# Kernel optimization log

Measured on AMD Instinct MI355X. Metric: run time of the kernel, lower is better.

The kernel has to match this reference:

```python
import jax, jax.numpy as jnp
import numpy as np

T, D, H, E, K = 4096, 1024, 2048, 8, 2  # tokens, model dim, expert hidden, n_experts, top_k
AUX_COEF = 0.01


def setup_inputs() -> dict:
    key = jax.random.key(0)
    ks = jax.random.split(key, 8)
    sd = lambda fan_in: 1.0 / np.sqrt(fan_in)
    x = jax.random.normal(ks[0], (T, D), jnp.float32)
    Wr = jax.random.normal(ks[1], (E, D), jnp.float32) * sd(D)      # router (no bias)
    w1 = jax.random.normal(ks[2], (E, H, D), jnp.float32) * sd(D)   # stacked up-proj
    w2 = jax.random.normal(ks[3], (E, D, H), jnp.float32) * sd(H)   # stacked down-proj
    w3 = jax.random.normal(ks[4], (E, H, D), jnp.float32) * sd(D)   # stacked gate-proj
    w1s = jax.random.normal(ks[5], (H, D), jnp.float32) * sd(D)     # shared expert
    w2s = jax.random.normal(ks[6], (D, H), jnp.float32) * sd(H)
    w3s = jax.random.normal(ks[7], (H, D), jnp.float32) * sd(D)
    return dict(x=x, Wr=Wr, w1=w1, w2=w2, w3=w3, w1s=w1s, w2s=w2s, w3s=w3s)


def _gelu(v):
    return jax.nn.gelu(v, approximate=False)  # torch F.gelu default = exact erf


def reference(x, Wr, w1, w2, w3, w1s, w2s, w3s):
    n_tok = x.shape[0]
    router_out = x @ Wr.T                                   # [T, E]
    router_probs = jax.nn.softmax(router_out, axis=-1)
    _, topk_idx = jax.lax.top_k(router_out, K)              # [T, K]
    topk_probs, _ = jax.lax.top_k(router_probs, K)          # top-k of probs (same order)

    # auxiliary load-balance loss (first-choice density * mean prob)
    expert_mask = jax.nn.one_hot(topk_idx[:, 0], E, dtype=jnp.float32)
    density = expert_mask.mean(axis=0)
    aux_loss = AUX_COEF * jnp.sum(density * router_probs.mean(axis=0)) * E

    # combine weights C[t, e] = sum of routed probs for expert e at token t
    C = jnp.zeros((n_tok, E), x.dtype).at[
        jnp.arange(n_tok)[:, None], topk_idx
    ].add(topk_probs)

    # dense per-expert SwiGLU-style FFN, combined by C (equal math to
    # sort-based dispatch + scatter_add in the original)
    h = _gelu(jnp.einsum('td,ehd->teh', x, w1)) * jnp.einsum('td,ehd->teh', x, w3)
    ye = jnp.einsum('teh,edh->ted', h, w2)                  # [T, E, D]
    out = jnp.einsum('ted,te->td', ye, C)

    # shared expert (always active)
    out = out + (_gelu(x @ w1s.T) * (x @ w3s.T)) @ w2s.T
    return out, aux_loss
```

## Files before the change

### kernel.cpp

```cpp
#include <hip/hip_runtime.h>
#include <hip/hip_bf16.h>
#include <cstdint>

#define T_TOK 4096
#define DMODEL 1024
#define HDIM 2048

typedef short bf16x8 __attribute__((ext_vector_type(8)));
typedef float f32x4 __attribute__((ext_vector_type(4)));
typedef uint32_t u32x4 __attribute__((ext_vector_type(4)));

#define WAITVM(N) asm volatile("s_waitcnt vmcnt(" #N ")" ::: "memory")
#define BARX() asm volatile("s_barrier" ::: "memory")

__device__ __forceinline__ uint32_t cvt_pk_bf16(float lo, float hi) {
  uint32_t d;
  asm("v_cvt_pk_bf16_f32 %0, %1, %2" : "=v"(d) : "v"(lo), "v"(hi));
  return d;
}
__device__ __forceinline__ unsigned short f2bf(float f) {
  uint32_t d;
  asm("v_cvt_pk_bf16_f32 %0, %1, %1" : "=v"(d) : "v"(f));
  return (unsigned short)d;
}
__device__ __forceinline__ float bf2f(unsigned short u) {
  return __uint_as_float((uint32_t)u << 16);
}
__device__ __forceinline__ float gelu_fast(float v) {
  float z = v * 0.70710678118654752f;
  float az = fabsf(z);
  float t = __frcp_rn(1.0f + 0.3275911f * az);
  float poly = ((((1.061405429f * t - 1.453152027f) * t + 1.421413741f) * t
                 - 0.284496736f) * t + 0.254829592f) * t;
  float er = 1.0f - poly * __expf(-z * z);
  er = (z < 0.f) ? -er : er;
  return 0.5f * v * (1.0f + er);
}
__device__ __forceinline__ void gload16(const void* g, void* lds) {
  __builtin_amdgcn_global_load_lds((const __attribute__((address_space(1))) void*)g,
                                   (__attribute__((address_space(3))) void*)lds, 16, 0, 0);
}
__device__ __forceinline__ u32x4 pk8(const float* s) {
  float4 v0 = ((const float4*)s)[0], v1 = ((const float4*)s)[1];
  u32x4 p = {cvt_pk_bf16(v0.x, v0.y), cvt_pk_bf16(v0.z, v0.w),
             cvt_pk_bf16(v1.x, v1.y), cvt_pk_bf16(v1.z, v1.w)};
  return p;
}
__device__ __forceinline__ int xcd_remap(int d, int nblk) {
  int q = nblk >> 3, r = nblk & 7, xc = d & 7, i = d >> 3;
  return (xc < r ? xc * (q + 1) : r * (q + 1) + (xc - r) * q) + i;
}

__global__ __launch_bounds__(256) void prep1_kernel(
    const float* __restrict__ x, const float* __restrict__ Wr,
    const float* __restrict__ w1, const float* __restrict__ w3,
    const float* __restrict__ w1s, const float* __restrict__ w3s,
    short* __restrict__ wB,
    int* __restrict__ cursor, int* __restrict__ cnt1,
    float* __restrict__ psum, int* __restrict__ perm,
    int* __restrict__ tokpos, float* __restrict__ wtok,
    short* __restrict__ xb) {
  __shared__ float sP[8];
  int bid = blockIdx.x, tid = threadIdx.x;

  if (bid < 1024) {
    int id0 = bid * 256 + tid;
#pragma unroll
    for (int it = 0; it < 18; ++it) {
      int id = id0 + it * 262144;
      int e = id >> 19, rem = id & 524287;
      int nf = rem >> 11, k32 = (rem >> 6) & 31, ln = rem & 63;
      int h = (nf >> 1) * 16 + (ln & 15);
      size_t so = (size_t)h * DMODEL + k32 * 32 + (ln >> 4) * 8;
      const float* src = (nf & 1)
          ? ((e < 8) ? w3 + (size_t)e * 2097152 + so : w3s + so)
          : ((e < 8) ? w1 + (size_t)e * 2097152 + so : w1s + so);
      *(u32x4*)(wB + (size_t)id * 8) = pk8(src);
    }
    return;
  }

  if (tid < 8) sP[tid] = 0.f;
  __syncthreads();

  int lane = tid & 63, wid = tid >> 6;
  int t = (bid - 1024) * 4 + wid;
  float acc[8] = {0.f, 0.f, 0.f, 0.f, 0.f, 0.f, 0.f, 0.f};
  const float4* x4 = (const float4*)(x + (size_t)t * DMODEL);
  const float4* W4 = (const float4*)Wr;
#pragma unroll
  for (int it = 0; it < 4; ++it) {
    float4 xv = x4[it * 64 + lane];
    uint2 pk = {cvt_pk_bf16(xv.x, xv.y), cvt_pk_bf16(xv.z, xv.w)};
    *(uint2*)(xb + (size_t)t * DMODEL + it * 256 + lane * 4) = pk;
#pragma unroll
    for (int e = 0; e < 8; ++e) {
      float4 wv = W4[e * 256 + it * 64 + lane];
      acc[e] += xv.x * wv.x + xv.y * wv.y + xv.z * wv.z + xv.w * wv.w;
    }
  }
#pragma unroll
  for (int e = 0; e < 8; ++e)
    for (int off = 32; off; off >>= 1) acc[e] += __shfl_xor(acc[e], off);

  float mx = acc[0];
#pragma unroll
  for (int e = 1; e < 8; ++e) mx = fmaxf(mx, acc[e]);
  float ex[8], s = 0.f;
#pragma unroll
  for (int e = 0; e < 8; ++e) { ex[e] = expf(acc[e] - mx); s += ex[e]; }
  float inv = 1.f / s;
  int e0 = 0;
#pragma unroll
  for (int e = 1; e < 8; ++e) if (acc[e] > acc[e0]) e0 = e;
  int e1 = (e0 == 0) ? 1 : 0;
#pragma unroll
  for (int e = 0; e < 8; ++e) if (e != e0 && acc[e] > acc[e1]) e1 = e;

  if (lane == 0) {
#pragma unroll
    for (int e = 0; e < 8; ++e) atomicAdd(&sP[e], ex[e] * inv);
    atomicAdd(&cnt1[e0], 1);
    int s0 = atomicAdd(&cursor[e0], 1);
    perm[e0 * 4096 + s0] = t;
    int s1 = atomicAdd(&cursor[e1], 1);
    perm[e1 * 4096 + s1] = t;
    tokpos[2 * t] = (e0 << 12) | s0;
    tokpos[2 * t + 1] = (e1 << 12) | s1;
    wtok[2 * t] = ex[e0] * inv;
    wtok[2 * t + 1] = ex[e1] * inv;
  }
  __syncthreads();
  if (tid < 8) atomicAdd(&psum[tid], sP[tid]);
}

__global__ void finalize_kernel(const int* __restrict__ cursor,
                                const int* __restrict__ cnt1,
                                const float* __restrict__ psum,
                                int* __restrict__ base,
                                int* __restrict__ work128, int* __restrict__ n128,
                                int* __restrict__ work256, int* __restrict__ n256,
                                float* __restrict__ aux_out) {
  if (threadIdx.x == 0) {
    int b = 0, a1 = 0, a2 = 0;
    for (int e = 0; e < 9; ++e) {
      int c = (e < 8) ? cursor[e] : 4096;
      base[e] = b;
      int t1 = (c + 127) >> 7;
      for (int mt = 0; mt < t1; ++mt) work128[a1++] = (e << 8) | mt;
      int t2 = (c + 255) >> 8;
      for (int mt = 0; mt < t2; ++mt) work256[a2++] = (e << 8) | mt;
      b += t2 << 8;
    }
    *n128 = a1; *n256 = a2;
    float aux = 0.f;
    for (int e = 0; e < 8; ++e)
      aux += ((float)cnt1[e] * (1.f / T_TOK)) * (psum[e] * (1.f / T_TOK));
    aux_out[0] = 0.01f * 8.f * aux;
  }
}

__global__ __launch_bounds__(256, 4) void gemm_upgate_f(
    const short* __restrict__ xb, const short* __restrict__ wB,
    const float* __restrict__ w2, const float* __restrict__ w2s,
    short* __restrict__ wd,
    const int* __restrict__ cursor, const int* __restrict__ base,
    const int* __restrict__ work, const int* __restrict__ nwork,
    const int* __restrict__ perm, unsigned short* __restrict__ hbuf) {
  __shared__ short lds[16384];

  if (blockIdx.x >= 3328) {
    int id0 = (blockIdx.x - 3328) * 256 + threadIdx.x;
#pragma unroll
    for (int it = 0; it < 18; ++it) {
      int id = id0 + it * 131072;
      int e = id >> 18, rem = id & 262143;
      int d16 = rem >> 12, h32 = (rem >> 6) & 63, ln = rem & 63;
      size_t so = (size_t)(d16 * 16 + (ln & 15)) * HDIM + h32 * 32 + (ln >> 4) * 8;
      const float* s2 = (e < 8) ? w2 + (size_t)e * 2097152 + so : w2s + so;
      *(u32x4*)(wd + (size_t)id * 8) = pk8(s2);
    }
    return;
  }

  int nblk = *nwork * 32;
  int d = blockIdx.x;
  if (d >= nblk) return;
  int o = xcd_remap(d, nblk);
  int y = o >> 5, nt = o & 31;
  int wk = work[y];
  int e = wk >> 8, mt = wk & 255;
  int cnt = (e < 8) ? cursor[e] : 4096;
  int hb = base[e];
  const short* wE = wB + (size_t)e * 4194304;

  int tid = threadIdx.x, lane = tid & 63, wid = tid >> 6;
  int fr = lane & 15, q4r = lane >> 4;
  int wm = wid >> 1, wn = wid & 1;

  size_t aOff[2], bOff[2];
#pragma unroll
  for (int c = 0; c < 2; ++c) {
    int g = c * 4 + wid;
    int slot = mt * 128 + g * 16 + fr;
    int tok = (e == 8) ? slot : ((slot < cnt) ? perm[e * 4096 + slot] : 0);
    aOff[c] = (size_t)tok * DMODEL + q4r * 8;
    bOff[c] = (size_t)(nt * 8 + g) * 32 * 512 + lane * 8;
  }

  auto stage = [&](int b, int t) {
#pragma unroll
    for (int c = 0; c < 2; ++c) {
      int g = c * 4 + wid;
      gload16(xb + aOff[c] + t * 32, &lds[b * 8192 + g * 512 + lane * 8]);
      gload16(wE + bOff[c] + (size_t)t * 512,
              &lds[b * 8192 + 4096 + g * 512 + lane * 8]);
    }
  };

  f32x4 acc[4][4] = {};

  auto compute = [&](int b) {
    bf16x8 af[4], bf[4];
#pragma unroll
    for (int m = 0; m < 4; ++m)
      af[m] = *(const bf16x8*)&lds[b * 8192 + (wm * 4 + m) * 512 + lane * 8];
#pragma unroll
    for (int n = 0; n < 4; ++n)
      bf[n] = *(const bf16x8*)&lds[b * 8192 + 4096 + (wn * 4 + n) * 512 + lane * 8];
    __builtin_amdgcn_s_setprio(1);
#pragma unroll
    for (int m = 0; m < 4; ++m)
#pragma unroll
      for (int n = 0; n < 4; ++n)
        acc[m][n] = __builtin_amdgcn_mfma_f32_16x16x32_bf16(af[m], bf[n], acc[m][n], 0, 0, 0);
    __builtin_amdgcn_s_setprio(0);
  };

  stage(0, 0);
  __syncthreads();
  int b = 0;
#pragma unroll 1
  for (int t = 0; t < 32; ++t) {
    if (t < 31) stage(b ^ 1, t + 1);
    compute(b);
    __syncthreads();
    b ^= 1;
  }

#pragma unroll
  for (int m = 0; m < 4; ++m) {
#pragma unroll
    for (int p = 0; p < 2; ++p) {
      f32x4 u = acc[m][2 * p], g = acc[m][2 * p + 1];
      int hcol = (nt * 4 + wn * 2 + p) * 16 + fr;
#pragma unroll
      for (int j = 0; j < 4; ++j) {
        int sl = mt * 128 + wm * 64 + m * 16 + q4r * 4 + j;
        float hv = (sl < cnt) ? gelu_fast(u[j]) * g[j] : 0.f;
        hbuf[(size_t)(hb + sl) * HDIM + hcol] = f2bf(hv);
      }
    }
  }
}

__global__ __launch_bounds__(512) void gemm_down8(
    const unsigned short* __restrict__ hbuf, const short* __restrict__ wd,
    const int* __restrict__ base,
    const int* __restrict__ work, const int* __restrict__ nwork,
    unsigned short* __restrict__ yb) {
  int y = blockIdx.y;
  if (y >= *nwork) return;
  int wk = work[y];
  int e = wk >> 8, mt = wk & 255, nt = blockIdx.x;
  int hb = base[e];
  const short* wdE = wd + (size_t)e * 2097152;

  __shared__ short lds[65536];

  int tid = threadIdx.x, lane = tid & 63, wid = tid >> 6;
  int wm = wid >> 2, wn = wid & 3;
  int fr = lane & 15, q4r = lane >> 4;

  size_t aOff[2];
#pragma unroll
  for (int c = 0; c < 2; ++c)
    aOff[c] = (size_t)(hb + mt * 256 + (c * 8 + wid) * 16 + fr) * HDIM + q4r * 8;
  size_t bOff[2];
#pragma unroll
  for (int c = 0; c < 2; ++c)
    bOff[c] = ((size_t)(nt * 16 + c * 8 + wid) * 64) * 512 + lane * 8;

#define DWN_STAGE_A(tt, k32)                                                   \
  { int bb_ = ((tt) & 1) * 32768;                                              \
    gload16(hbuf + aOff[0] + (tt) * 64 + (k32) * 32,                           \
            &lds[bb_ + ((k32) * 16 + wid) * 512 + lane * 8]);                  \
    gload16(hbuf + aOff[1] + (tt) * 64 + (k32) * 32,                           \
            &lds[bb_ + ((k32) * 16 + 8 + wid) * 512 + lane * 8]); }
#define DWN_STAGE_B(tt, k32)                                                   \
  { int bb_ = ((tt) & 1) * 32768;                                              \
    gload16(wdE + bOff[0] + (size_t)((tt) * 2 + (k32)) * 512,                  \
            &lds[bb_ + 16384 + ((k32) * 16 + wid) * 512 + lane * 8]);          \
    gload16(wdE + bOff[1] + (size_t)((tt) * 2 + (k32)) * 512,                  \
            &lds[bb_ + 16384 + ((k32) * 16 + 8 + wid) * 512 + lane * 8]); }
#define DWN_READA(k32, mh)                                                     \
  { _Pragma("unroll") for (int i = 0; i < 4; ++i)                              \
      af[i] = *(const bf16x8*)&lds[bb + ((k32) * 16 + wm * 8 + (mh) * 4 + i) * \
                                       512 + lane * 8]; }
#define DWN_READB(k32)                                                         \
  { _Pragma("unroll") for (int n = 0; n < 4; ++n)                              \
      bf[n] = *(const bf16x8*)&lds[bb + 16384 + ((k32) * 16 + wn * 4 + n) *    \
                                       512 + lane * 8]; }
#define DWN_MFMA(mh)                                                           \
  { __builtin_amdgcn_s_setprio(1);                                             \
    _Pragma("unroll") for (int i = 0; i < 4; ++i)                              \
      _Pragma("unroll") for (int n = 0; n < 4; ++n)                            \
        acc[(mh) * 4 + i][n] = __builtin_amdgcn_mfma_f32_16x16x32_bf16(        \
            af[i], bf[n], acc[(mh) * 4 + i][n], 0, 0, 0);                      \
    __builtin_amdgcn_s_setprio(0); }

  f32x4 acc[8][4] = {};
  bf16x8 af[4], bf[4];

  DWN_STAGE_A(0, 0); DWN_STAGE_B(0, 0); DWN_STAGE_A(0, 1); DWN_STAGE_B(0, 1);
  WAITVM(4); BARX();

#pragma unroll 1
  for (int t = 0; t < 31; ++t) {
    const int bb = (t & 1) * 32768;
    DWN_READA(0, 0); DWN_READB(0); DWN_STAGE_A(t + 1, 0);
    BARX(); DWN_MFMA(0); BARX();
    DWN_READA(0, 1); DWN_STAGE_B(t + 1, 0);
    BARX(); DWN_MFMA(1); WAITVM(4); BARX();
    DWN_READA(1, 0); DWN_READB(1); DWN_STAGE_A(t + 1, 1);
    BARX(); DWN_MFMA(0); BARX();
    DWN_READA(1, 1); DWN_STAGE_B(t + 1, 1);
    BARX(); DWN_MFMA(1); WAITVM(4); BARX();
  }
  {
    const int bb = 32768;
    DWN_READA(0, 0); DWN_READB(0); BARX(); DWN_MFMA(0); BARX();
    DWN_READA(0, 1); BARX(); DWN_MFMA(1); WAITVM(0); BARX();
    DWN_READA(1, 0); DWN_READB(1); BARX(); DWN_MFMA(0); BARX();
    DWN_READA(1, 1); DWN_MFMA(1);
  }

#pragma unroll
  for (int m = 0; m < 8; ++m) {
#pragma unroll
    for (int n = 0; n < 4; ++n) {
      int col = (nt * 16 + wn * 4 + n) * 16 + fr;
      f32x4 a = acc[m][n];
#pragma unroll
      for (int j = 0; j < 4; ++j) {
        int row = mt * 256 + wm * 128 + m * 16 + q4r * 4 + j;
        yb[(size_t)(hb + row) * DMODEL + col] = f2bf(a[j]);
      }
    }
  }
}

__global__ __launch_bounds__(256) void gather_kernel(
    const unsigned short* __restrict__ yb, const int* __restrict__ tokpos,
    const float* __restrict__ wtok, const int* __restrict__ base,
    float* __restrict__ out) {
  int t = blockIdx.x, c4 = threadIdx.x;
  int p0 = tokpos[2 * t], p1 = tokpos[2 * t + 1];
  float w0 = wtok[2 * t], w1 = wtok[2 * t + 1];
  size_t r0 = (size_t)(base[p0 >> 12] + (p0 & 4095)) * DMODEL;
  size_t r1 = (size_t)(base[p1 >> 12] + (p1 & 4095)) * DMODEL;
  size_t rs = (size_t)(base[8] + t) * DMODEL;
  ushort4 v0 = *(const ushort4*)(yb + r0 + c4 * 4);
  ushort4 v1 = *(const ushort4*)(yb + r1 + c4 * 4);
  ushort4 vs = *(const ushort4*)(yb + rs + c4 * 4);
  float4 o;
  o.x = w0 * bf2f(v0.x) + w1 * bf2f(v1.x) + bf2f(vs.x);
  o.y = w0 * bf2f(v0.y) + w1 * bf2f(v1.y) + bf2f(vs.y);
  o.z = w0 * bf2f(v0.z) + w1 * bf2f(v1.z) + bf2f(vs.z);
  o.w = w0 * bf2f(v0.w) + w1 * bf2f(v1.w) + bf2f(vs.w);
  *(float4*)(out + (size_t)t * DMODEL + c4 * 4) = o;
}

extern "C" void kernel_launch(void* const* d_in, const int* in_sizes, int n_in,
                              void* d_out, int out_size, void* d_ws, size_t ws_size,
                              hipStream_t stream) {
  const float* x   = (const float*)d_in[0];
  const float* Wr  = (const float*)d_in[1];
  const float* w1  = (const float*)d_in[2];
  const float* w2  = (const float*)d_in[3];
  const float* w3  = (const float*)d_in[4];
  const float* w1s = (const float*)d_in[5];
  const float* w2s = (const float*)d_in[6];
  const float* w3s = (const float*)d_in[7];
  float* out = (float*)d_out;

  char* ws = (char*)d_ws;
  const size_t HBUF_OFF = 0;
  const size_t XB_OFF   = 58720256;
  const size_t WB_OFF   = XB_OFF + 8388608;
  const size_t WD_OFF   = WB_OFF + 75497472;
  const size_t PERM_OFF = WD_OFF + 37748736;
  const size_t TP_OFF   = PERM_OFF + 131072;
  const size_t WT_OFF   = TP_OFF + 32768;
  const size_t CTRL_OFF = WT_OFF + 32768;
  const size_t W128_OFF = CTRL_OFF + 256;
  const size_t W256_OFF = W128_OFF + 512;

  unsigned short* hbuf = (unsigned short*)(ws + HBUF_OFF);
  short* xb = (short*)(ws + XB_OFF);
  short* wB = (short*)(ws + WB_OFF);
  short* wd = (short*)(ws + WD_OFF);
  unsigned short* yb = (unsigned short*)(ws + WB_OFF);
  int*   perm   = (int*)(ws + PERM_OFF);
  int*   tokpos = (int*)(ws + TP_OFF);
  float* wtok   = (float*)(ws + WT_OFF);
  int*   cursor = (int*)(ws + CTRL_OFF);
  int*   cnt1   = (int*)(ws + CTRL_OFF + 64);
  float* psum   = (float*)(ws + CTRL_OFF + 128);
  int*   base   = (int*)(ws + CTRL_OFF + 192);
  int*   n128   = (int*)(ws + CTRL_OFF + 236);
  int*   n256   = (int*)(ws + CTRL_OFF + 240);
  int*   work128 = (int*)(ws + W128_OFF);
  int*   work256 = (int*)(ws + W256_OFF);

  hipMemsetAsync(ws + CTRL_OFF, 0, 256, stream);

  prep1_kernel<<<2048, 256, 0, stream>>>(x, Wr, w1, w3, w1s, w3s, wB,
                                         cursor, cnt1, psum, perm,
                                         tokpos, wtok, xb);
  finalize_kernel<<<1, 64, 0, stream>>>(cursor, cnt1, psum, base,
                                        work128, n128, work256, n256,
                                        out + (size_t)T_TOK * DMODEL);
  gemm_upgate_f<<<3840, 256, 0, stream>>>(xb, wB, w2, w2s, wd,
                                          cursor, base, work128, n128,
                                          perm, hbuf);
  gemm_down8<<<dim3(4, 64), 512, 0, stream>>>(hbuf, wd, base, work256, n256, yb);
  gather_kernel<<<4096, 256, 0, stream>>>(yb, tokpos, wtok, base, out);
}
```

Measured before the change: 377.0 us.

## Load fp32 up/gate weights directly in GEMM, converting to bf16 in registers

Drops the separate pre-pass that repacked w1/w3 (and the shared-expert copies) into a bf16 buffer. The up/gate GEMM now streams fp32 weights straight into LDS and packs them to bf16 fragments just before the MFMA. The w2 repack moves from the tail of the up/gate launch into prep1. This saves a write and reread of about 75MB of bf16 weights, but doubles the weight bytes each GEMM tile loads, raises LDS use, and lowers the occupancy bound to 3.

```diff
diff --git a/kernel.cpp b/kernel.cpp
--- a/kernel.cpp
+++ b/kernel.cpp
@@ -46,6 +46,12 @@
              cvt_pk_bf16(v1.x, v1.y), cvt_pk_bf16(v1.z, v1.w)};
   return p;
 }
+__device__ __forceinline__ bf16x8 pkfrag(f32x4 a, f32x4 b) {
+  union { u32x4 u; bf16x8 s; } r;
+  r.u = (u32x4){cvt_pk_bf16(a[0], a[1]), cvt_pk_bf16(a[2], a[3]),
+                cvt_pk_bf16(b[0], b[1]), cvt_pk_bf16(b[2], b[3])};
+  return r.s;
+}
 __device__ __forceinline__ int xcd_remap(int d, int nblk) {
   int q = nblk >> 3, r = nblk & 7, xc = d & 7, i = d >> 3;
   return (xc < r ? xc * (q + 1) : r * (q + 1) + (xc - r) * q) + i;
@@ -53,9 +59,8 @@
 
 __global__ __launch_bounds__(256) void prep1_kernel(
     const float* __restrict__ x, const float* __restrict__ Wr,
-    const float* __restrict__ w1, const float* __restrict__ w3,
-    const float* __restrict__ w1s, const float* __restrict__ w3s,
-    short* __restrict__ wB,
+    const float* __restrict__ w2, const float* __restrict__ w2s,
+    short* __restrict__ wd,
     int* __restrict__ cursor, int* __restrict__ cnt1,
     float* __restrict__ psum, int* __restrict__ perm,
     int* __restrict__ tokpos, float* __restrict__ wtok,
@@ -66,16 +71,13 @@
   if (bid < 1024) {
     int id0 = bid * 256 + tid;
 #pragma unroll
-    for (int it = 0; it < 18; ++it) {
+    for (int it = 0; it < 9; ++it) {
       int id = id0 + it * 262144;
-      int e = id >> 19, rem = id & 524287;
-      int nf = rem >> 11, k32 = (rem >> 6) & 31, ln = rem & 63;
-      int h = (nf >> 1) * 16 + (ln & 15);
-      size_t so = (size_t)h * DMODEL + k32 * 32 + (ln >> 4) * 8;
-      const float* src = (nf & 1)
-          ? ((e < 8) ? w3 + (size_t)e * 2097152 + so : w3s + so)
-          : ((e < 8) ? w1 + (size_t)e * 2097152 + so : w1s + so);
-      *(u32x4*)(wB + (size_t)id * 8) = pk8(src);
+      int e = id >> 18, rem = id & 262143;
+      int d16 = rem >> 12, h32 = (rem >> 6) & 63, ln = rem & 63;
+      size_t so = (size_t)(d16 * 16 + (ln & 15)) * HDIM + h32 * 32 + (ln >> 4) * 8;
+      const float* s2 = (e < 8) ? w2 + (size_t)e * 2097152 + so : w2s + so;
+      *(u32x4*)(wd + (size_t)id * 8) = pk8(s2);
     }
     return;
   }
@@ -160,29 +162,13 @@
   }
 }
 
-__global__ __launch_bounds__(256, 4) void gemm_upgate_f(
-    const short* __restrict__ xb, const short* __restrict__ wB,
-    const float* __restrict__ w2, const float* __restrict__ w2s,
-    short* __restrict__ wd,
+__global__ __launch_bounds__(256, 3) void gemm_upgate(
+    const short* __restrict__ xb,
+    const float* __restrict__ w1, const float* __restrict__ w3,
+    const float* __restrict__ w1s, const float* __restrict__ w3s,
     const int* __restrict__ cursor, const int* __restrict__ base,
     const int* __restrict__ work, const int* __restrict__ nwork,
     const int* __restrict__ perm, unsigned short* __restrict__ hbuf) {
-  __shared__ short lds[16384];
-
-  if (blockIdx.x >= 3328) {
-    int id0 = (blockIdx.x - 3328) * 256 + threadIdx.x;
-#pragma unroll
-    for (int it = 0; it < 18; ++it) {
-      int id = id0 + it * 131072;
-      int e = id >> 18, rem = id & 262143;
-      int d16 = rem >> 12, h32 = (rem >> 6) & 63, ln = rem & 63;
-      size_t so = (size_t)(d16 * 16 + (ln & 15)) * HDIM + h32 * 32 + (ln >> 4) * 8;
-      const float* s2 = (e < 8) ? w2 + (size_t)e * 2097152 + so : w2s + so;
-      *(u32x4*)(wd + (size_t)id * 8) = pk8(s2);
-    }
-    return;
-  }
-
   int nblk = *nwork * 32;
   int d = blockIdx.x;
   if (d >= nblk) return;
@@ -192,42 +178,56 @@
   int e = wk >> 8, mt = wk & 255;
   int cnt = (e < 8) ? cursor[e] : 4096;
   int hb = base[e];
-  const short* wE = wB + (size_t)e * 4194304;
+
+  __shared__ short lds[24576];
 
   int tid = threadIdx.x, lane = tid & 63, wid = tid >> 6;
   int fr = lane & 15, q4r = lane >> 4;
   int wm = wid >> 1, wn = wid & 1;
 
-  size_t aOff[2], bOff[2];
+  size_t aOff[2];
 #pragma unroll
   for (int c = 0; c < 2; ++c) {
     int g = c * 4 + wid;
     int slot = mt * 128 + g * 16 + fr;
     int tok = (e == 8) ? slot : ((slot < cnt) ? perm[e * 4096 + slot] : 0);
     aOff[c] = (size_t)tok * DMODEL + q4r * 8;
-    bOff[c] = (size_t)(nt * 8 + g) * 32 * 512 + lane * 8;
+  }
+  const float* bSrc[2];
+#pragma unroll
+  for (int c = 0; c < 2; ++c) {
+    int nf = nt * 8 + c * 4 + wid;
+    const float* M = (nf & 1) ? ((e < 8) ? w3 + (size_t)e * 2097152 : w3s)
+                              : ((e < 8) ? w1 + (size_t)e * 2097152 : w1s);
+    bSrc[c] = M + (size_t)((nf >> 1) * 16 + fr) * DMODEL + q4r * 8;
   }
 
   auto stage = [&](int b, int t) {
+    int bs = b * 12288;
 #pragma unroll
     for (int c = 0; c < 2; ++c) {
       int g = c * 4 + wid;
-      gload16(xb + aOff[c] + t * 32, &lds[b * 8192 + g * 512 + lane * 8]);
-      gload16(wE + bOff[c] + (size_t)t * 512,
-              &lds[b * 8192 + 4096 + g * 512 + lane * 8]);
+      gload16(xb + aOff[c] + t * 32, &lds[bs + g * 512 + lane * 8]);
+      gload16(bSrc[c] + t * 32,     &lds[bs + 4096 + (g * 2 + 0) * 512 + lane * 8]);
+      gload16(bSrc[c] + t * 32 + 4, &lds[bs + 4096 + (g * 2 + 1) * 512 + lane * 8]);
     }
   };
 
   f32x4 acc[4][4] = {};
 
   auto compute = [&](int b) {
+    int bs = b * 12288;
     bf16x8 af[4], bf[4];
 #pragma unroll
     for (int m = 0; m < 4; ++m)
-      af[m] = *(const bf16x8*)&lds[b * 8192 + (wm * 4 + m) * 512 + lane * 8];
-#pragma unroll
-    for (int n = 0; n < 4; ++n)
-      bf[n] = *(const bf16x8*)&lds[b * 8192 + 4096 + (wn * 4 + n) * 512 + lane * 8];
+      af[m] = *(const bf16x8*)&lds[bs + (wm * 4 + m) * 512 + lane * 8];
+#pragma unroll
+    for (int n = 0; n < 4; ++n) {
+      int lg = wn * 4 + n;
+      f32x4 h0 = *(const f32x4*)&lds[bs + 4096 + (lg * 2 + 0) * 512 + lane * 8];
+      f32x4 h1 = *(const f32x4*)&lds[bs + 4096 + (lg * 2 + 1) * 512 + lane * 8];
+      bf[n] = pkfrag(h0, h1);
+    }
     __builtin_amdgcn_s_setprio(1);
 #pragma unroll
     for (int m = 0; m < 4; ++m)
@@ -397,8 +397,8 @@
   char* ws = (char*)d_ws;
   const size_t HBUF_OFF = 0;
   const size_t XB_OFF   = 58720256;
-  const size_t WB_OFF   = XB_OFF + 8388608;
-  const size_t WD_OFF   = WB_OFF + 75497472;
+  const size_t YB_OFF   = XB_OFF + 8388608;
+  const size_t WD_OFF   = YB_OFF + 29360128;
   const size_t PERM_OFF = WD_OFF + 37748736;
   const size_t TP_OFF   = PERM_OFF + 131072;
   const size_t WT_OFF   = TP_OFF + 32768;
@@ -408,9 +408,8 @@
 
   unsigned short* hbuf = (unsigned short*)(ws + HBUF_OFF);
   short* xb = (short*)(ws + XB_OFF);
-  short* wB = (short*)(ws + WB_OFF);
+  unsigned short* yb = (unsigned short*)(ws + YB_OFF);
   short* wd = (short*)(ws + WD_OFF);
-  unsigned short* yb = (unsigned short*)(ws + WB_OFF);
   int*   perm   = (int*)(ws + PERM_OFF);
   int*   tokpos = (int*)(ws + TP_OFF);
   float* wtok   = (float*)(ws + WT_OFF);
@@ -425,15 +424,15 @@
 
   hipMemsetAsync(ws + CTRL_OFF, 0, 256, stream);
 
-  prep1_kernel<<<2048, 256, 0, stream>>>(x, Wr, w1, w3, w1s, w3s, wB,
+  prep1_kernel<<<2048, 256, 0, stream>>>(x, Wr, w2, w2s, wd,
                                          cursor, cnt1, psum, perm,
                                          tokpos, wtok, xb);
   finalize_kernel<<<1, 64, 0, stream>>>(cursor, cnt1, psum, base,
                                         work128, n128, work256, n256,
                                         out + (size_t)T_TOK * DMODEL);
-  gemm_upgate_f<<<3840, 256, 0, stream>>>(xb, wB, w2, w2s, wd,
-                                          cursor, base, work128, n128,
-                                          perm, hbuf);
+  gemm_upgate<<<3328, 256, 0, stream>>>(xb, w1, w3, w1s, w3s,
+                                        cursor, base, work128, n128,
+                                        perm, hbuf);
   gemm_down8<<<dim3(4, 64), 512, 0, stream>>>(hbuf, wd, base, work256, n256, yb);
   gather_kernel<<<4096, 256, 0, stream>>>(yb, tokpos, wtok, base, out);
 }
```

After: 498.3 us. +32.2%, slower.

## Store bf16 weights in natural row-major layout and move w2 conversion into prep

Applied to the files above, without the earlier changes.

Weight conversion no longer writes an MFMA-fragment-tiled layout. It writes plain row-major bf16 copies of w1, w3 and w2, and the down-projection weight conversion moves from the tail of the up/gate GEMM launch into the prep kernel. The GEMMs now compute B-tile addresses from row-major strides, so conversion writes become fully contiguous and the up/gate launch carries only GEMM blocks. In exchange, GEMM global loads into LDS now stride across rows instead of reading contiguous pre-tiled chunks, which may reduce load coalescing.

```diff
diff --git a/kernel.cpp b/kernel.cpp
--- a/kernel.cpp
+++ b/kernel.cpp
@@ -51,11 +51,15 @@
   return (xc < r ? xc * (q + 1) : r * (q + 1) + (xc - r) * q) + i;
 }
 
+#define ESTRIDE 2097152
+#define RCHUNK 2359296
+
 __global__ __launch_bounds__(256) void prep1_kernel(
     const float* __restrict__ x, const float* __restrict__ Wr,
     const float* __restrict__ w1, const float* __restrict__ w3,
     const float* __restrict__ w1s, const float* __restrict__ w3s,
-    short* __restrict__ wB,
+    const float* __restrict__ w2, const float* __restrict__ w2s,
+    short* __restrict__ wb,
     int* __restrict__ cursor, int* __restrict__ cnt1,
     float* __restrict__ psum, int* __restrict__ perm,
     int* __restrict__ tokpos, float* __restrict__ wtok,
@@ -63,19 +67,25 @@
   __shared__ float sP[8];
   int bid = blockIdx.x, tid = threadIdx.x;
 
-  if (bid < 1024) {
+  if (bid < 1536) {
     int id0 = bid * 256 + tid;
 #pragma unroll
     for (int it = 0; it < 18; ++it) {
-      int id = id0 + it * 262144;
-      int e = id >> 19, rem = id & 524287;
-      int nf = rem >> 11, k32 = (rem >> 6) & 31, ln = rem & 63;
-      int h = (nf >> 1) * 16 + (ln & 15);
-      size_t so = (size_t)h * DMODEL + k32 * 32 + (ln >> 4) * 8;
-      const float* src = (nf & 1)
-          ? ((e < 8) ? w3 + (size_t)e * 2097152 + so : w3s + so)
-          : ((e < 8) ? w1 + (size_t)e * 2097152 + so : w1s + so);
-      *(u32x4*)(wB + (size_t)id * 8) = pk8(src);
+      int id = id0 + it * 393216;
+      const float* src;
+      if (id < RCHUNK) {
+        src = (id < ESTRIDE) ? w1 + (size_t)id * 8
+                             : w1s + (size_t)(id - ESTRIDE) * 8;
+      } else if (id < 2 * RCHUNK) {
+        int l = id - RCHUNK;
+        src = (l < ESTRIDE) ? w3 + (size_t)l * 8
+                            : w3s + (size_t)(l - ESTRIDE) * 8;
+      } else {
+        int l = id - 2 * RCHUNK;
+        src = (l < ESTRIDE) ? w2 + (size_t)l * 8
+                            : w2s + (size_t)(l - ESTRIDE) * 8;
+      }
+      *(u32x4*)(wb + (size_t)id * 8) = pk8(src);
     }
     return;
   }
@@ -84,7 +94,7 @@
   __syncthreads();
 
   int lane = tid & 63, wid = tid >> 6;
-  int t = (bid - 1024) * 4 + wid;
+  int t = (bid - 1536) * 4 + wid;
   float acc[8] = {0.f, 0.f, 0.f, 0.f, 0.f, 0.f, 0.f, 0.f};
   const float4* x4 = (const float4*)(x + (size_t)t * DMODEL);
   const float4* W4 = (const float4*)Wr;
@@ -160,29 +170,12 @@
   }
 }
 
-__global__ __launch_bounds__(256, 4) void gemm_upgate_f(
-    const short* __restrict__ xb, const short* __restrict__ wB,
-    const float* __restrict__ w2, const float* __restrict__ w2s,
-    short* __restrict__ wd,
+__global__ __launch_bounds__(256, 4) void gemm_upgate(
+    const short* __restrict__ xb,
+    const short* __restrict__ w1b, const short* __restrict__ w3b,
     const int* __restrict__ cursor, const int* __restrict__ base,
     const int* __restrict__ work, const int* __restrict__ nwork,
     const int* __restrict__ perm, unsigned short* __restrict__ hbuf) {
-  __shared__ short lds[16384];
-
-  if (blockIdx.x >= 3328) {
-    int id0 = (blockIdx.x - 3328) * 256 + threadIdx.x;
-#pragma unroll
-    for (int it = 0; it < 18; ++it) {
-      int id = id0 + it * 131072;
-      int e = id >> 18, rem = id & 262143;
-      int d16 = rem >> 12, h32 = (rem >> 6) & 63, ln = rem & 63;
-      size_t so = (size_t)(d16 * 16 + (ln & 15)) * HDIM + h32 * 32 + (ln >> 4) * 8;
-      const float* s2 = (e < 8) ? w2 + (size_t)e * 2097152 + so : w2s + so;
-      *(u32x4*)(wd + (size_t)id * 8) = pk8(s2);
-    }
-    return;
-  }
-
   int nblk = *nwork * 32;
   int d = blockIdx.x;
   if (d >= nblk) return;
@@ -192,20 +185,25 @@
   int e = wk >> 8, mt = wk & 255;
   int cnt = (e < 8) ? cursor[e] : 4096;
   int hb = base[e];
-  const short* wE = wB + (size_t)e * 4194304;
+
+  __shared__ short lds[16384];
 
   int tid = threadIdx.x, lane = tid & 63, wid = tid >> 6;
   int fr = lane & 15, q4r = lane >> 4;
   int wm = wid >> 1, wn = wid & 1;
 
-  size_t aOff[2], bOff[2];
+  size_t aOff[2];
+  const short* bSrc[2];
 #pragma unroll
   for (int c = 0; c < 2; ++c) {
     int g = c * 4 + wid;
     int slot = mt * 128 + g * 16 + fr;
     int tok = (e == 8) ? slot : ((slot < cnt) ? perm[e * 4096 + slot] : 0);
     aOff[c] = (size_t)tok * DMODEL + q4r * 8;
-    bOff[c] = (size_t)(nt * 8 + g) * 32 * 512 + lane * 8;
+    int nf = nt * 8 + g;
+    const short* M = (nf & 1) ? w3b + (size_t)e * ESTRIDE
+                              : w1b + (size_t)e * ESTRIDE;
+    bSrc[c] = M + (size_t)((nf >> 1) * 16 + fr) * DMODEL + q4r * 8;
   }
 
   auto stage = [&](int b, int t) {
@@ -213,8 +211,7 @@
     for (int c = 0; c < 2; ++c) {
       int g = c * 4 + wid;
       gload16(xb + aOff[c] + t * 32, &lds[b * 8192 + g * 512 + lane * 8]);
-      gload16(wE + bOff[c] + (size_t)t * 512,
-              &lds[b * 8192 + 4096 + g * 512 + lane * 8]);
+      gload16(bSrc[c] + t * 32, &lds[b * 8192 + 4096 + g * 512 + lane * 8]);
     }
   };
 
@@ -265,7 +262,7 @@
 }
 
 __global__ __launch_bounds__(512) void gemm_down8(
-    const unsigned short* __restrict__ hbuf, const short* __restrict__ wd,
+    const unsigned short* __restrict__ hbuf, const short* __restrict__ w2b,
     const int* __restrict__ base,
     const int* __restrict__ work, const int* __restrict__ nwork,
     unsigned short* __restrict__ yb) {
@@ -274,7 +271,7 @@
   int wk = work[y];
   int e = wk >> 8, mt = wk & 255, nt = blockIdx.x;
   int hb = base[e];
-  const short* wdE = wd + (size_t)e * 2097152;
+  const short* w2bE = w2b + (size_t)e * ESTRIDE;
 
   __shared__ short lds[65536];
 
@@ -282,14 +279,12 @@
   int wm = wid >> 2, wn = wid & 3;
   int fr = lane & 15, q4r = lane >> 4;
 
-  size_t aOff[2];
-#pragma unroll
-  for (int c = 0; c < 2; ++c)
+  size_t aOff[2], bOff[2];
+#pragma unroll
+  for (int c = 0; c < 2; ++c) {
     aOff[c] = (size_t)(hb + mt * 256 + (c * 8 + wid) * 16 + fr) * HDIM + q4r * 8;
-  size_t bOff[2];
-#pragma unroll
-  for (int c = 0; c < 2; ++c)
-    bOff[c] = ((size_t)(nt * 16 + c * 8 + wid) * 64) * 512 + lane * 8;
+    bOff[c] = (size_t)((nt * 16 + c * 8 + wid) * 16 + fr) * HDIM + q4r * 8;
+  }
 
 #define DWN_STAGE_A(tt, k32)                                                   \
   { int bb_ = ((tt) & 1) * 32768;                                              \
@@ -299,9 +294,9 @@
             &lds[bb_ + ((k32) * 16 + 8 + wid) * 512 + lane * 8]); }
 #define DWN_STAGE_B(tt, k32)                                                   \
   { int bb_ = ((tt) & 1) * 32768;                                              \
-    gload16(wdE + bOff[0] + (size_t)((tt) * 2 + (k32)) * 512,                  \
+    gload16(w2bE + bOff[0] + (tt) * 64 + (k32) * 32,                           \
             &lds[bb_ + 16384 + ((k32) * 16 + wid) * 512 + lane * 8]);          \
-    gload16(wdE + bOff[1] + (size_t)((tt) * 2 + (k32)) * 512,                  \
+    gload16(w2bE + bOff[1] + (tt) * 64 + (k32) * 32,                           \
             &lds[bb_ + 16384 + ((k32) * 16 + 8 + wid) * 512 + lane * 8]); }
 #define DWN_READA(k32, mh)                                                     \
   { _Pragma("unroll") for (int i = 0; i < 4; ++i)                              \
@@ -398,8 +393,9 @@
   const size_t HBUF_OFF = 0;
   const size_t XB_OFF   = 58720256;
   const size_t WB_OFF   = XB_OFF + 8388608;
-  const size_t WD_OFF   = WB_OFF + 75497472;
-  const size_t PERM_OFF = WD_OFF + 37748736;
+  const size_t W3B_OFF  = WB_OFF + 37748736;
+  const size_t W2B_OFF  = W3B_OFF + 37748736;
+  const size_t PERM_OFF = W2B_OFF + 37748736;
   const size_t TP_OFF   = PERM_OFF + 131072;
   const size_t WT_OFF   = TP_OFF + 32768;
   const size_t CTRL_OFF = WT_OFF + 32768;
@@ -407,9 +403,10 @@
   const size_t W256_OFF = W128_OFF + 512;
 
   unsigned short* hbuf = (unsigned short*)(ws + HBUF_OFF);
-  short* xb = (short*)(ws + XB_OFF);
-  short* wB = (short*)(ws + WB_OFF);
-  short* wd = (short*)(ws + WD_OFF);
+  short* xb  = (short*)(ws + XB_OFF);
+  short* w1b = (short*)(ws + WB_OFF);
+  short* w3b = (short*)(ws + W3B_OFF);
+  short* w2b = (short*)(ws + W2B_OFF);
   unsigned short* yb = (unsigned short*)(ws + WB_OFF);
   int*   perm   = (int*)(ws + PERM_OFF);
   int*   tokpos = (int*)(ws + TP_OFF);
@@ -425,15 +422,14 @@
 
   hipMemsetAsync(ws + CTRL_OFF, 0, 256, stream);
 
-  prep1_kernel<<<2048, 256, 0, stream>>>(x, Wr, w1, w3, w1s, w3s, wB,
-                                         cursor, cnt1, psum, perm,
+  prep1_kernel<<<2560, 256, 0, stream>>>(x, Wr, w1, w3, w1s, w3s, w2, w2s,
+                                         w1b, cursor, cnt1, psum, perm,
                                          tokpos, wtok, xb);
   finalize_kernel<<<1, 64, 0, stream>>>(cursor, cnt1, psum, base,
                                         work128, n128, work256, n256,
                                         out + (size_t)T_TOK * DMODEL);
-  gemm_upgate_f<<<3840, 256, 0, stream>>>(xb, wB, w2, w2s, wd,
-                                          cursor, base, work128, n128,
-                                          perm, hbuf);
-  gemm_down8<<<dim3(4, 64), 512, 0, stream>>>(hbuf, wd, base, work256, n256, yb);
+  gemm_upgate<<<3328, 256, 0, stream>>>(xb, w1b, w3b, cursor, base,
+                                        work128, n128, perm, hbuf);
+  gemm_down8<<<dim3(4, 64), 512, 0, stream>>>(hbuf, w2b, base, work256, n256, yb);
   gather_kernel<<<4096, 256, 0, stream>>>(yb, tokpos, wtok, base, out);
 }
```

New measurement: 445.8 us. +18.3%, slower.
